# Kernel tuning notes

Measured on AMD Instinct MI355X. Metric: run time of the kernel, lower is better.

## Reference

```python
import jax, jax.numpy as jnp
import numpy as np

N_TOKENS, D_MODEL, D_FF, TOP_K, N_EXPERTS = 8192, 1024, 4096, 2, 8
CAPACITY_FACTOR = 2.0  # static capacity; with uniform routing overflow prob is ~0 (>40 sigma)


def setup_inputs() -> dict:
    key = jax.random.key(0)
    k_x, k_idx, k_w, k1, k2, k3 = jax.random.split(key, 6)
    std_in = (1.0 / 3.0) ** 0.5 / (D_MODEL ** 0.5)   # fan_in = d_model for w1, w2
    std_out = (1.0 / 3.0) ** 0.5 / (D_FF ** 0.5)      # fan_in = d_ff for w3
    x = jax.random.normal(k_x, (N_TOKENS, D_MODEL), jnp.float32)
    expert_indices = jax.random.randint(k_idx, (N_TOKENS, TOP_K), 0, N_EXPERTS)
    expert_weights = jax.random.uniform(k_w, (N_TOKENS, TOP_K), jnp.float32)
    w1 = jax.random.truncated_normal(k1, -2.0, 2.0, (N_EXPERTS, D_MODEL, D_FF), jnp.float32) * std_in
    w2 = jax.random.truncated_normal(k2, -2.0, 2.0, (N_EXPERTS, D_MODEL, D_FF), jnp.float32) * std_in
    w3 = jax.random.truncated_normal(k3, -2.0, 2.0, (N_EXPERTS, D_FF, D_MODEL), jnp.float32) * std_out
    return {"x": x, "expert_indices": expert_indices, "expert_weights": expert_weights,
            "w1": w1, "w2": w2, "w3": w3}


def reference(x, expert_indices, expert_weights, w1, w2, w3):
    n_tokens, d_model = x.shape
    n_experts = w1.shape[0]
    top_k = expert_indices.shape[1]
    total = n_tokens * top_k
    cap = int(CAPACITY_FACTOR * total / n_experts)  # static per-expert capacity (stands in for dynamic max_count)

    flat_experts = expert_indices.reshape(-1)                      # [total]
    flat_weights = expert_weights.reshape(-1)                      # [total]
    token_indices = jnp.repeat(jnp.arange(n_tokens), top_k)        # [total], matches expand+reshape

    order = jnp.argsort(flat_experts, stable=True)
    sorted_tok = token_indices[order]
    sorted_eid = flat_experts[order]
    sorted_wts = flat_weights[order]

    counts = jnp.bincount(flat_experts, length=n_experts)
    seg_starts = jnp.concatenate([jnp.zeros((1,), counts.dtype), jnp.cumsum(counts)[:-1]])
    positions = jnp.arange(total) - seg_starts[sorted_eid]         # slot within expert segment
    valid = positions < cap
    pos_c = jnp.minimum(positions, cap)                             # overflow goes to dump row `cap`

    # dispatch: [n_experts, cap+1, d_model] (last row is dump slot)
    padded = jnp.zeros((n_experts, cap + 1, d_model), x.dtype).at[sorted_eid, pos_c].set(x[sorted_tok])

    # per-expert SwiGLU FFN (grouped GEMMs)
    gate = jax.nn.silu(jnp.einsum('ecd,edf->ecf', padded, w1))
    value = jnp.einsum('ecd,edf->ecf', padded, w2)
    expert_out = jnp.einsum('ecf,efd->ecd', gate * value, w3)       # [n_experts, cap+1, d_model]

    gathered = expert_out[sorted_eid, pos_c]                        # [total, d_model]
    gathered = gathered * jnp.where(valid, sorted_wts, 0.0)[:, None]

    return jnp.zeros((n_tokens, d_model), x.dtype).at[sorted_tok].add(gathered)
```

## Files before the change

kernel.cpp:

```cpp
#include <hip/hip_runtime.h>
#include <stdint.h>

#define N_TOKENS  8192
#define D_MODEL   1024
#define D_FF      4096
#define TOP_K     2
#define N_EXPERTS 8
#define TOTAL_SLOTS (N_TOKENS * TOP_K)
#define CAP       4096
#define ROWS_PAD  (TOTAL_SLOTS + 128)

typedef unsigned short u16;
typedef __attribute__((ext_vector_type(4))) float f32x4;
typedef __attribute__((ext_vector_type(8))) short bf16x8;

__device__ __forceinline__ float bf2f(u16 u) {
  union { unsigned int i; float f; } v; v.i = ((unsigned int)u) << 16; return v.f;
}
__device__ __forceinline__ u16 f2bf(float f) {
  union { float f; unsigned int i; } v; v.f = f;
  unsigned int u = v.i;
  return (u16)((u + 0x7FFFu + ((u >> 16) & 1u)) >> 16);
}

__device__ __forceinline__ void gld_lds16(const void* g, void* l) {
  __builtin_amdgcn_global_load_lds(
      (const __attribute__((address_space(1))) unsigned int*)g,
      (__attribute__((address_space(3))) unsigned int*)l,
      16, 0, 0);
}

__global__ __launch_bounds__(256) void k_route(const int* __restrict__ eidx,
                                               int* __restrict__ info,
                                               int* __restrict__ row_of_slot,
                                               int* __restrict__ tok_of_row) {
  __shared__ int s_total[N_EXPERTS];
  __shared__ int s_start[N_EXPERTS];
  __shared__ int s_base[N_EXPERTS];
  __shared__ int s_wcnt[4][N_EXPERTS];
  const int t = threadIdx.x;
  const int lane = t & 63;
  const int w = t >> 6;

  if (t < N_EXPERTS) { s_total[t] = 0; s_base[t] = 0; }
  __syncthreads();

  for (int c = 0; c < TOTAL_SLOTS / 256; ++c) {
    int e = eidx[c * 256 + t];
    atomicAdd(&s_total[e], 1);
  }
  __syncthreads();

  if (t == 0) {
    int off = 0;
    for (int e = 0; e < N_EXPERTS; ++e) {
      int placed = s_total[e] < CAP ? s_total[e] : CAP;
      s_start[e] = off;
      info[e] = placed;
      info[N_EXPERTS + e] = off;
      off += placed;
    }
    info[2 * N_EXPERTS] = off;
  }
  __syncthreads();

  for (int c = 0; c < TOTAL_SLOTS / 256; ++c) {
    int s = c * 256 + t;
    int e = eidx[s];
    unsigned long long mymask = 0;
    for (int ee = 0; ee < N_EXPERTS; ++ee) {
      unsigned long long m = __ballot(e == ee);
      if (ee == e) mymask = m;
      if (lane == 0) s_wcnt[w][ee] = __popcll(m);
    }
    int rank_in_wave = __popcll(mymask & ((1ULL << lane) - 1ULL));
    __syncthreads();
    int prior = 0;
    for (int ww = 0; ww < w; ++ww) prior += s_wcnt[ww][e];
    int pos = s_base[e] + prior + rank_in_wave;
    int row = (pos < CAP) ? (s_start[e] + pos) : -1;
    row_of_slot[s] = row;
    if (row >= 0) tok_of_row[row] = s >> 1;
    __syncthreads();
    if (t < N_EXPERTS) {
      int tot = 0;
      for (int ww = 0; ww < 4; ++ww) tot += s_wcnt[ww][t];
      s_base[t] += tot;
    }
    __syncthreads();
  }
}

__global__ __launch_bounds__(256) void k_transpose(const float* __restrict__ in,
                                                   u16* __restrict__ out,
                                                   int R, int C) {
  __shared__ float tile[64][65];
  const int e = blockIdx.z;
  in  += (size_t)e * R * C;
  out += (size_t)e * R * C;
  const int c0 = blockIdx.x * 64;
  const int r0 = blockIdx.y * 64;
  const int tx = threadIdx.x & 15, ty = threadIdx.x >> 4;

  #pragma unroll
  for (int rr = 0; rr < 4; ++rr) {
    int r = ty + rr * 16;
    float4 v = *(const float4*)&in[(size_t)(r0 + r) * C + c0 + tx * 4];
    tile[r][tx * 4 + 0] = v.x; tile[r][tx * 4 + 1] = v.y;
    tile[r][tx * 4 + 2] = v.z; tile[r][tx * 4 + 3] = v.w;
  }
  __syncthreads();
  #pragma unroll
  for (int rr = 0; rr < 4; ++rr) {
    int oc = ty + rr * 16;
    ushort4 o;
    o.x = f2bf(tile[tx * 4 + 0][oc]);
    o.y = f2bf(tile[tx * 4 + 1][oc]);
    o.z = f2bf(tile[tx * 4 + 2][oc]);
    o.w = f2bf(tile[tx * 4 + 3][oc]);
    *(ushort4*)&out[(size_t)(c0 + oc) * R + r0 + tx * 4] = o;
  }
}

__global__ __launch_bounds__(256) void k_dispatch(const float* __restrict__ x,
                                                  const int* __restrict__ tok_of_row,
                                                  const int* __restrict__ info,
                                                  u16* __restrict__ Xd) {
  const int r = blockIdx.x;
  const int t = threadIdx.x;
  const int total = info[2 * N_EXPERTS];
  if (r >= total) {
    ushort4 z = {0, 0, 0, 0};
    *(ushort4*)&Xd[(size_t)r * D_MODEL + t * 4] = z;
    return;
  }
  int tok = tok_of_row[r];
  float4 v = *(const float4*)&x[(size_t)tok * D_MODEL + t * 4];
  ushort4 o;
  o.x = f2bf(v.x); o.y = f2bf(v.y); o.z = f2bf(v.z); o.w = f2bf(v.w);
  *(ushort4*)&Xd[(size_t)r * D_MODEL + t * 4] = o;
}

__global__ __launch_bounds__(256, 2) void k_ffn1(const u16* __restrict__ Xd,
                                                 const u16* __restrict__ W1t,
                                                 const u16* __restrict__ W2t,
                                                 u16* __restrict__ H,
                                                 const int* __restrict__ info) {
  const int e = blockIdx.z;
  const int count = info[e];
  const int row0 = blockIdx.y * 128;
  if (row0 >= count) return;
  const int start = info[N_EXPERTS + e];
  const int col0 = blockIdx.x * 128;

  __shared__ u16 lsA[128 * 64];
  __shared__ u16 lsB1[128 * 64];
  __shared__ u16 lsB2[128 * 64];

  const int t = threadIdx.x, lane = t & 63, wid = t >> 6;
  const int wr = wid >> 1, wc = wid & 1;

  const u16* gA  = Xd  + (size_t)(start + row0) * D_MODEL;
  const u16* gB1 = W1t + (size_t)e * D_FF * D_MODEL + (size_t)col0 * D_MODEL;
  const u16* gB2 = W2t + (size_t)e * D_FF * D_MODEL + (size_t)col0 * D_MODEL;

  f32x4 accG[4][4] = {};
  f32x4 accV[4][4] = {};

  const int srow = wid * 8 + (lane >> 3);
  const int skk  = (((lane & 7) ^ ((lane >> 3) & 7)) * 8);
  const int rk0 = (((0 * 4 + (lane >> 4)) ^ (lane & 7)) * 8);
  const int rk1 = (((1 * 4 + (lane >> 4)) ^ (lane & 7)) * 8);

  for (int k0 = 0; k0 < D_MODEL; k0 += 64) {
    __syncthreads();
    #pragma unroll
    for (int i = 0; i < 4; ++i) {
      int r = i * 32 + srow;
      int lbase = (i * 32 + wid * 8) * 64;
      gld_lds16(gA  + (size_t)r * D_MODEL + k0 + skk, &lsA[lbase]);
      gld_lds16(gB1 + (size_t)r * D_MODEL + k0 + skk, &lsB1[lbase]);
      gld_lds16(gB2 + (size_t)r * D_MODEL + k0 + skk, &lsB2[lbase]);
    }
    __syncthreads();
    #pragma unroll
    for (int kk = 0; kk < 2; ++kk) {
      const int rk = kk ? rk1 : rk0;
      bf16x8 a[4];
      #pragma unroll
      for (int m = 0; m < 4; ++m)
        a[m] = *(const bf16x8*)&lsA[(wr * 64 + m * 16 + (lane & 15)) * 64 + rk];
      #pragma unroll
      for (int n = 0; n < 4; ++n) {
        bf16x8 b1 = *(const bf16x8*)&lsB1[(wc * 64 + n * 16 + (lane & 15)) * 64 + rk];
        bf16x8 b2 = *(const bf16x8*)&lsB2[(wc * 64 + n * 16 + (lane & 15)) * 64 + rk];
        #pragma unroll
        for (int m = 0; m < 4; ++m) {
          accG[m][n] = __builtin_amdgcn_mfma_f32_16x16x32_bf16(a[m], b1, accG[m][n], 0, 0, 0);
          accV[m][n] = __builtin_amdgcn_mfma_f32_16x16x32_bf16(a[m], b2, accV[m][n], 0, 0, 0);
        }
      }
    }
  }

  const int rmax = count - row0;
  const size_t hbase = (size_t)(start + row0);
  #pragma unroll
  for (int m = 0; m < 4; ++m) {
    #pragma unroll
    for (int j = 0; j < 4; ++j) {
      int rit = wr * 64 + m * 16 + (lane >> 4) * 4 + j;
      if (rit < rmax) {
        #pragma unroll
        for (int n = 0; n < 4; ++n) {
          float g = accG[m][n][j];
          float v = accV[m][n][j];
          float h = g * v / (1.0f + __expf(-g));
          H[(hbase + rit) * D_FF + col0 + wc * 64 + n * 16 + (lane & 15)] = f2bf(h);
        }
      }
    }
  }
}

__global__ __launch_bounds__(256) void k_ffn2(const u16* __restrict__ Hbuf,
                                              const u16* __restrict__ W3t,
                                              u16* __restrict__ Y,
                                              const int* __restrict__ info) {
  const int e = blockIdx.z;
  const int count = info[e];
  const int row0 = blockIdx.y * 128;
  if (row0 >= count) return;
  const int start = info[N_EXPERTS + e];
  const int col0 = blockIdx.x * 128;

  __shared__ u16 lsA[128 * 64];
  __shared__ u16 lsB[128 * 64];

  const int t = threadIdx.x, lane = t & 63, wid = t >> 6;
  const int wr = wid >> 1, wc = wid & 1;

  const u16* gA = Hbuf + (size_t)(start + row0) * D_FF;
  const u16* gB = W3t + (size_t)e * D_MODEL * D_FF + (size_t)col0 * D_FF;

  f32x4 acc[4][4] = {};

  const int srow = wid * 8 + (lane >> 3);
  const int skk  = (((lane & 7) ^ ((lane >> 3) & 7)) * 8);
  const int rk0 = (((0 * 4 + (lane >> 4)) ^ (lane & 7)) * 8);
  const int rk1 = (((1 * 4 + (lane >> 4)) ^ (lane & 7)) * 8);

  for (int k0 = 0; k0 < D_FF; k0 += 64) {
    __syncthreads();
    #pragma unroll
    for (int i = 0; i < 4; ++i) {
      int r = i * 32 + srow;
      int lbase = (i * 32 + wid * 8) * 64;
      gld_lds16(gA + (size_t)r * D_FF + k0 + skk, &lsA[lbase]);
      gld_lds16(gB + (size_t)r * D_FF + k0 + skk, &lsB[lbase]);
    }
    __syncthreads();
    #pragma unroll
    for (int kk = 0; kk < 2; ++kk) {
      const int rk = kk ? rk1 : rk0;
      bf16x8 a[4];
      #pragma unroll
      for (int m = 0; m < 4; ++m)
        a[m] = *(const bf16x8*)&lsA[(wr * 64 + m * 16 + (lane & 15)) * 64 + rk];
      #pragma unroll
      for (int n = 0; n < 4; ++n) {
        bf16x8 b = *(const bf16x8*)&lsB[(wc * 64 + n * 16 + (lane & 15)) * 64 + rk];
        #pragma unroll
        for (int m = 0; m < 4; ++m)
          acc[m][n] = __builtin_amdgcn_mfma_f32_16x16x32_bf16(a[m], b, acc[m][n], 0, 0, 0);
      }
    }
  }

  const int rmax = count - row0;
  const size_t ybase = (size_t)(start + row0);
  #pragma unroll
  for (int m = 0; m < 4; ++m) {
    #pragma unroll
    for (int j = 0; j < 4; ++j) {
      int rit = wr * 64 + m * 16 + (lane >> 4) * 4 + j;
      if (rit < rmax) {
        #pragma unroll
        for (int n = 0; n < 4; ++n)
          Y[(ybase + rit) * D_MODEL + col0 + wc * 64 + n * 16 + (lane & 15)] = f2bf(acc[m][n][j]);
      }
    }
  }
}

__global__ __launch_bounds__(256) void k_combine(const u16* __restrict__ Y,
                                                 const int* __restrict__ row_of_slot,
                                                 const float* __restrict__ ew,
                                                 float* __restrict__ out) {
  const int tok = blockIdx.x;
  const int c = threadIdx.x * 4;
  const int r0 = row_of_slot[tok * 2 + 0];
  const int r1 = row_of_slot[tok * 2 + 1];
  const float w0 = ew[tok * 2 + 0];
  const float w1 = ew[tok * 2 + 1];
  float a0 = 0.f, a1 = 0.f, a2 = 0.f, a3 = 0.f;
  if (r0 >= 0) {
    ushort4 y = *(const ushort4*)&Y[(size_t)r0 * D_MODEL + c];
    a0 = w0 * bf2f(y.x); a1 = w0 * bf2f(y.y); a2 = w0 * bf2f(y.z); a3 = w0 * bf2f(y.w);
  }
  if (r1 >= 0) {
    ushort4 y = *(const ushort4*)&Y[(size_t)r1 * D_MODEL + c];
    a0 += w1 * bf2f(y.x); a1 += w1 * bf2f(y.y); a2 += w1 * bf2f(y.z); a3 += w1 * bf2f(y.w);
  }
  float4 o; o.x = a0; o.y = a1; o.z = a2; o.w = a3;
  *(float4*)&out[(size_t)tok * D_MODEL + c] = o;
}

extern "C" void kernel_launch(void* const* d_in, const int* in_sizes, int n_in,
                              void* d_out, int out_size, void* d_ws, size_t ws_size,
                              hipStream_t stream) {
  const float* x  = (const float*)d_in[0];
  const int*   ei = (const int*)d_in[1];
  const float* ew = (const float*)d_in[2];
  const float* w1 = (const float*)d_in[3];
  const float* w2 = (const float*)d_in[4];
  const float* w3 = (const float*)d_in[5];
  float* out = (float*)d_out;

  char* ws = (char*)d_ws;
  size_t off = 0;
  auto alloc = [&](size_t b) { char* p = ws + off; off += (b + 255) & ~(size_t)255; return p; };
  int* info        = (int*)alloc(256);
  int* row_of_slot = (int*)alloc(sizeof(int) * TOTAL_SLOTS);
  int* tok_of_row  = (int*)alloc(sizeof(int) * ROWS_PAD);
  u16* Xd  = (u16*)alloc((size_t)2 * ROWS_PAD * D_MODEL);
  u16* W1t = (u16*)alloc((size_t)2 * N_EXPERTS * D_FF * D_MODEL);
  u16* W2t = (u16*)alloc((size_t)2 * N_EXPERTS * D_FF * D_MODEL);
  u16* W3t = (u16*)alloc((size_t)2 * N_EXPERTS * D_FF * D_MODEL);
  u16* H   = (u16*)alloc((size_t)2 * ROWS_PAD * D_FF);
  u16* Y   = (u16*)alloc((size_t)2 * ROWS_PAD * D_MODEL);

  k_route<<<1, 256, 0, stream>>>(ei, info, row_of_slot, tok_of_row);
  k_transpose<<<dim3(D_FF / 64, D_MODEL / 64, N_EXPERTS), 256, 0, stream>>>(w1, W1t, D_MODEL, D_FF);
  k_transpose<<<dim3(D_FF / 64, D_MODEL / 64, N_EXPERTS), 256, 0, stream>>>(w2, W2t, D_MODEL, D_FF);
  k_transpose<<<dim3(D_MODEL / 64, D_FF / 64, N_EXPERTS), 256, 0, stream>>>(w3, W3t, D_FF, D_MODEL);
  k_dispatch<<<ROWS_PAD, 256, 0, stream>>>(x, tok_of_row, info, Xd);
  k_ffn1<<<dim3(D_FF / 128, CAP / 128, N_EXPERTS), 256, 0, stream>>>(Xd, W1t, W2t, H, info);
  k_ffn2<<<dim3(D_MODEL / 128, CAP / 128, N_EXPERTS), 256, 0, stream>>>(H, W3t, Y, info);
  k_combine<<<N_TOKENS, 256, 0, stream>>>(Y, row_of_slot, ew, out);
}
```

Baseline: 744.0 us.

## Parallelize routing with block-wide ballot prefix and merge weight transposes

The routing kernel now runs 1024 threads, and each thread loads all of its expert ids up front. Per-wave expert counts for every round come from ballots and are stored in shared memory, and a single serial prefix pass over those counts yields every slot position. This removes the 64 sequential rounds, each of which needed three barriers, that the old single-block routing loop spent. The three weight-transpose launches are also merged into one launch with a 24-deep z grid, which removes launch overhead and lets the three weight tensors be processed concurrently. The routing kernel is still a single block, and its results stay deterministic and stable-ordered.

```diff
diff --git a/kernel.cpp b/kernel.cpp
--- a/kernel.cpp
+++ b/kernel.cpp
@@ -30,76 +30,91 @@
       16, 0, 0);
 }
 
-__global__ __launch_bounds__(256) void k_route(const int* __restrict__ eidx,
-                                               int* __restrict__ info,
-                                               int* __restrict__ row_of_slot,
-                                               int* __restrict__ tok_of_row) {
-  __shared__ int s_total[N_EXPERTS];
+#define RT_THREADS 1024
+#define RT_ROUNDS  (TOTAL_SLOTS / RT_THREADS)
+#define RT_WAVES   (RT_THREADS / 64)
+
+__global__ __launch_bounds__(RT_THREADS) void k_route(const int* __restrict__ eidx,
+                                                      int* __restrict__ info,
+                                                      int* __restrict__ row_of_slot,
+                                                      int* __restrict__ tok_of_row) {
+  __shared__ int s_wcnt[RT_ROUNDS][RT_WAVES][N_EXPERTS];
+  __shared__ int s_pbase[RT_ROUNDS][RT_WAVES][N_EXPERTS];
   __shared__ int s_start[N_EXPERTS];
-  __shared__ int s_base[N_EXPERTS];
-  __shared__ int s_wcnt[4][N_EXPERTS];
-  const int t = threadIdx.x;
-  const int lane = t & 63;
-  const int w = t >> 6;
-
-  if (t < N_EXPERTS) { s_total[t] = 0; s_base[t] = 0; }
+  const int t = threadIdx.x, lane = t & 63, w = t >> 6;
+
+  int e[RT_ROUNDS];
+  #pragma unroll
+  for (int c = 0; c < RT_ROUNDS; ++c) e[c] = eidx[c * RT_THREADS + t];
+
+  unsigned long long mym[RT_ROUNDS];
+  #pragma unroll
+  for (int c = 0; c < RT_ROUNDS; ++c) {
+    unsigned long long mm = 0;
+    #pragma unroll
+    for (int ee = 0; ee < N_EXPERTS; ++ee) {
+      unsigned long long m = __ballot(e[c] == ee);
+      if (e[c] == ee) mm = m;
+      if (lane == ee) s_wcnt[c][w][ee] = __popcll(m);
+    }
+    mym[c] = mm;
+  }
   __syncthreads();
 
-  for (int c = 0; c < TOTAL_SLOTS / 256; ++c) {
-    int e = eidx[c * 256 + t];
-    atomicAdd(&s_total[e], 1);
+  if (t < N_EXPERTS) {
+    int tot = 0;
+    for (int c = 0; c < RT_ROUNDS; ++c)
+      for (int ww = 0; ww < RT_WAVES; ++ww) {
+        s_pbase[c][ww][t] = tot;
+        tot += s_wcnt[c][ww][t];
+      }
+    s_start[t] = tot;
   }
   __syncthreads();
-
   if (t == 0) {
     int off = 0;
-    for (int e = 0; e < N_EXPERTS; ++e) {
-      int placed = s_total[e] < CAP ? s_total[e] : CAP;
-      s_start[e] = off;
-      info[e] = placed;
-      info[N_EXPERTS + e] = off;
+    for (int ee = 0; ee < N_EXPERTS; ++ee) {
+      int tot = s_start[ee];
+      int placed = tot < CAP ? tot : CAP;
+      info[ee] = placed;
+      info[N_EXPERTS + ee] = off;
+      s_start[ee] = off;
       off += placed;
     }
     info[2 * N_EXPERTS] = off;
   }
   __syncthreads();
 
-  for (int c = 0; c < TOTAL_SLOTS / 256; ++c) {
-    int s = c * 256 + t;
-    int e = eidx[s];
-    unsigned long long mymask = 0;
-    for (int ee = 0; ee < N_EXPERTS; ++ee) {
-      unsigned long long m = __ballot(e == ee);
-      if (ee == e) mymask = m;
-      if (lane == 0) s_wcnt[w][ee] = __popcll(m);
-    }
-    int rank_in_wave = __popcll(mymask & ((1ULL << lane) - 1ULL));
-    __syncthreads();
-    int prior = 0;
-    for (int ww = 0; ww < w; ++ww) prior += s_wcnt[ww][e];
-    int pos = s_base[e] + prior + rank_in_wave;
-    int row = (pos < CAP) ? (s_start[e] + pos) : -1;
+  #pragma unroll
+  for (int c = 0; c < RT_ROUNDS; ++c) {
+    const int s = c * RT_THREADS + t;
+    const int rank = __popcll(mym[c] & ((1ULL << lane) - 1ULL));
+    const int pos = s_pbase[c][w][e[c]] + rank;
+    const int row = (pos < CAP) ? (s_start[e[c]] + pos) : -1;
     row_of_slot[s] = row;
     if (row >= 0) tok_of_row[row] = s >> 1;
-    __syncthreads();
-    if (t < N_EXPERTS) {
-      int tot = 0;
-      for (int ww = 0; ww < 4; ++ww) tot += s_wcnt[ww][t];
-      s_base[t] += tot;
-    }
-    __syncthreads();
-  }
-}
-
-__global__ __launch_bounds__(256) void k_transpose(const float* __restrict__ in,
-                                                   u16* __restrict__ out,
-                                                   int R, int C) {
+  }
+}
+
+__global__ __launch_bounds__(256) void k_transpose_all(const float* __restrict__ w1,
+                                                       const float* __restrict__ w2,
+                                                       const float* __restrict__ w3,
+                                                       u16* __restrict__ W1t,
+                                                       u16* __restrict__ W2t,
+                                                       u16* __restrict__ W3t) {
   __shared__ float tile[64][65];
-  const int e = blockIdx.z;
+  const int z = blockIdx.z;
+  const int e = z & 7, which = z >> 3;
+  const float* in;
+  u16* out;
+  int R, C, c0, r0;
+  if (which == 0)      { in = w1; out = W1t; R = D_MODEL; C = D_FF; }
+  else if (which == 1) { in = w2; out = W2t; R = D_MODEL; C = D_FF; }
+  else                 { in = w3; out = W3t; R = D_FF;    C = D_MODEL; }
+  if (which == 2) { c0 = blockIdx.y * 64; r0 = blockIdx.x * 64; }
+  else            { c0 = blockIdx.x * 64; r0 = blockIdx.y * 64; }
   in  += (size_t)e * R * C;
   out += (size_t)e * R * C;
-  const int c0 = blockIdx.x * 64;
-  const int r0 = blockIdx.y * 64;
   const int tx = threadIdx.x & 15, ty = threadIdx.x >> 4;
 
   #pragma unroll
@@ -340,10 +355,8 @@
   u16* H   = (u16*)alloc((size_t)2 * ROWS_PAD * D_FF);
   u16* Y   = (u16*)alloc((size_t)2 * ROWS_PAD * D_MODEL);
 
-  k_route<<<1, 256, 0, stream>>>(ei, info, row_of_slot, tok_of_row);
-  k_transpose<<<dim3(D_FF / 64, D_MODEL / 64, N_EXPERTS), 256, 0, stream>>>(w1, W1t, D_MODEL, D_FF);
-  k_transpose<<<dim3(D_FF / 64, D_MODEL / 64, N_EXPERTS), 256, 0, stream>>>(w2, W2t, D_MODEL, D_FF);
-  k_transpose<<<dim3(D_MODEL / 64, D_FF / 64, N_EXPERTS), 256, 0, stream>>>(w3, W3t, D_FF, D_MODEL);
+  k_route<<<1, RT_THREADS, 0, stream>>>(ei, info, row_of_slot, tok_of_row);
+  k_transpose_all<<<dim3(64, 16, 24), 256, 0, stream>>>(w1, w2, w3, W1t, W2t, W3t);
   k_dispatch<<<ROWS_PAD, 256, 0, stream>>>(x, tok_of_row, info, Xd);
   k_ffn1<<<dim3(D_FF / 128, CAP / 128, N_EXPERTS), 256, 0, stream>>>(Xd, W1t, W2t, H, info);
   k_ffn2<<<dim3(D_MODEL / 128, CAP / 128, N_EXPERTS), 256, 0, stream>>>(H, W3t, Y, info);
```

Result: faster. 687.9 us, median of 2 (-7.5%).
